# Kernel tuning notes

Measured on AMD Instinct MI355X. Metric: run time of the kernel, lower is better.

## Reference

```python
import jax, jax.numpy as jnp
import numpy as np

B, H, S, D = 2, 16, 2048, 64
NEG = -1e9

def setup_inputs() -> dict:
    key = jax.random.key(0)
    kq, kk, kv, km = jax.random.split(key, 4)
    q = jax.random.normal(kq, (B, H, S, D), dtype=jnp.float32)
    k = jax.random.normal(kk, (B, H, S, D), dtype=jnp.float32)
    v = jax.random.normal(kv, (B, H, S, D), dtype=jnp.float32)
    mask = jax.random.randint(km, (S, S), 0, 2, dtype=jnp.int32)
    return {"q": q, "k": k, "v": v, "mask": mask}

def reference(q, k, v, mask):
    d_k = k.shape[-1]
    temp = jnp.sqrt(jnp.asarray(d_k, q.dtype))  # temperature=None -> sqrt(d_k)
    # scores: [B,H,S,S]
    scores = jnp.einsum('bhqd,bhkd->bhqk', q, k) / temp
    scores = jnp.where(mask == 0, jnp.asarray(NEG, scores.dtype), scores)
    attn = jax.nn.softmax(scores, axis=-1)
    output = jnp.einsum('bhqk,bhkd->bhqd', attn, v)
    return (output, attn)
```

## Files before the change

kernel.cpp:

```cpp
#include <hip/hip_runtime.h>
#include <stdint.h>

#define S 2048
#define D 64
#define NKT (S / 64)
#define SCALEF 0.125f

typedef __attribute__((ext_vector_type(8))) _Float16 half8;
typedef __attribute__((ext_vector_type(4))) float floatx4;
typedef __attribute__((ext_vector_type(4))) unsigned int uint32x4;

__device__ __forceinline__ float redsum16(float x) {
#pragma unroll
  for (int off = 8; off >= 1; off >>= 1) x += __shfl_xor(x, off, 16);
  return x;
}

__global__ __launch_bounds__(256) void conv_k_tiled(const float* __restrict__ k,
                                                    _Float16* __restrict__ kh) {
  __shared__ float tile[64][68];
  int bh = blockIdx.x >> 5;
  int kt = blockIdx.x & 31;
  const floatx4* src4 = (const floatx4*)(k + ((size_t)bh * S + (size_t)kt * 64) * D);
#pragma unroll
  for (int it = 0; it < 4; it++) {
    int idx = threadIdx.x + 256 * it;
    *(floatx4*)&tile[idx >> 4][(idx & 15) * 4] = src4[idx];
  }
  __syncthreads();
  half8* dst = (half8*)(kh + (size_t)(bh * 32 + kt) * 512 * 8);
#pragma unroll
  for (int it = 0; it < 2; it++) {
    int cl = threadIdx.x + 256 * it;
    int quad = cl & 3;
    int r = (cl >> 2) & 63;
    int ch = cl >> 8;
    const float* s = &tile[r][ch * 32 + quad * 8];
    half8 h;
#pragma unroll
    for (int j = 0; j < 8; j++) h[j] = (_Float16)s[j];
    dst[cl] = h;
  }
}

__global__ __launch_bounds__(256) void conv_v_tiled(const float* __restrict__ v,
                                                    _Float16* __restrict__ vt) {
  __shared__ float tile[64][68];
  int bh = blockIdx.x >> 5;
  int kt = blockIdx.x & 31;
  const floatx4* src4 = (const floatx4*)(v + ((size_t)bh * S + (size_t)kt * 64) * D);
#pragma unroll
  for (int it = 0; it < 4; it++) {
    int idx = threadIdx.x + 256 * it;
    *(floatx4*)&tile[idx >> 4][(idx & 15) * 4] = src4[idx];
  }
  __syncthreads();
  half8* dst = (half8*)(vt + (size_t)(bh * 32 + kt) * 512 * 8);
#pragma unroll
  for (int it = 0; it < 2; it++) {
    int cl = threadIdx.x + 256 * it;
    int quad = cl & 3;
    int d = (cl >> 2) & 63;
    int c2 = cl >> 8;
    int kb = c2 * 32 + quad * 8;
    half8 h;
#pragma unroll
    for (int j = 0; j < 8; j++) h[j] = (_Float16)tile[kb + j][d];
    dst[cl] = h;
  }
}

__global__ __launch_bounds__(256) void pack_mask_kernel(const int* __restrict__ mask,
                                                        uint32_t* __restrict__ mp) {
  int i = blockIdx.x * 256 + threadIdx.x;
  int r4 = i & 3;
  int c16 = (i >> 2) & 15;
  int quad = (i >> 6) & 3;
  int kt = (i >> 8) & 31;
  int rt = i >> 13;
  int row = rt * 16 + quad * 4 + r4;
  const int* p = mask + (size_t)row * S + kt * 64 + c16;
  uint32_t b0 = (uint32_t)(p[0] != 0);
  uint32_t b1 = (uint32_t)(p[16] != 0);
  uint32_t b2 = (uint32_t)(p[32] != 0);
  uint32_t b3 = (uint32_t)(p[48] != 0);
  mp[i] = b0 | (b1 << 8) | (b2 << 16) | (b3 << 24);
}

__global__ __launch_bounds__(256, 4) void attn_kernel(
    const float* __restrict__ q, const _Float16* __restrict__ kh,
    const _Float16* __restrict__ vt, const uint32_t* __restrict__ mp,
    float* __restrict__ out_o, float* __restrict__ out_attn) {
  const int bh = blockIdx.x >> 5;
  const int qt = blockIdx.x & 31;
  const int lane = threadIdx.x & 63;
  const int wid = threadIdx.x >> 6;
  const int c16 = lane & 15;
  const int quad = lane >> 4;
  const int rowbase = qt * 64 + wid * 16;

  half8 aq[2];
  {
    const float* qrow = q + ((size_t)bh * S + rowbase + c16) * D + quad * 8;
#pragma unroll
    for (int ch = 0; ch < 2; ch++) {
      const floatx4* p4 = (const floatx4*)(qrow + ch * 32);
      floatx4 f0 = p4[0];
      floatx4 f1 = p4[1];
      half8 h;
      h[0] = (_Float16)(f0[0] * SCALEF); h[1] = (_Float16)(f0[1] * SCALEF);
      h[2] = (_Float16)(f0[2] * SCALEF); h[3] = (_Float16)(f0[3] * SCALEF);
      h[4] = (_Float16)(f1[0] * SCALEF); h[5] = (_Float16)(f1[1] * SCALEF);
      h[6] = (_Float16)(f1[2] * SCALEF); h[7] = (_Float16)(f1[3] * SCALEF);
      aq[ch] = h;
    }
  }

  const _Float16* kbase = kh + ((size_t)bh * 32 * 512 + (size_t)(c16 * 4 + quad)) * 8;
  const _Float16* vbase = vt + ((size_t)bh * 32 * 512 + (size_t)(c16 * 4 + quad)) * 8;
  const uint32x4* mb4 = (const uint32x4*)mp + (size_t)(qt * 4 + wid) * 32 * 64 + lane;

  float l_part[4];
#pragma unroll
  for (int r = 0; r < 4; r++) l_part[r] = 0.0f;

#pragma unroll 1
  for (int kt = 0; kt < NKT; kt++) {
    floatx4 acc[4];
#pragma unroll
    for (int nt = 0; nt < 4; nt++) {
      floatx4 a = {0.0f, 0.0f, 0.0f, 0.0f};
#pragma unroll
      for (int ch = 0; ch < 2; ch++) {
        half8 b = *(const half8*)(kbase + ((size_t)kt * 512 + ch * 256 + nt * 64) * 8);
        a = __builtin_amdgcn_mfma_f32_16x16x32_f16(aq[ch], b, a, 0, 0, 0);
      }
      acc[nt] = a;
    }
    uint32x4 mm = mb4[(size_t)kt * 64];
#pragma unroll
    for (int r = 0; r < 4; r++) {
      uint32_t mb = mm[r];
#pragma unroll
      for (int nt = 0; nt < 4; nt++) {
        float p = ((mb >> (8 * nt)) & 1u) ? __expf(acc[nt][r]) : 0.0f;
        l_part[r] += p;
      }
    }
  }

  float inv_l[4];
#pragma unroll
  for (int r = 0; r < 4; r++) inv_l[r] = 1.0f / redsum16(l_part[r]);

  __shared__ __align__(16) _Float16 plds[2][4][16][72];
  floatx4 oacc[4];
#pragma unroll
  for (int nt = 0; nt < 4; nt++) oacc[nt] = (floatx4){0.0f, 0.0f, 0.0f, 0.0f};

  float* attn_base = out_attn + ((size_t)bh * S + rowbase + 4 * quad) * S + c16;

#pragma unroll 1
  for (int kt = 0; kt < NKT; kt++) {
    floatx4 acc[4];
#pragma unroll
    for (int nt = 0; nt < 4; nt++) {
      floatx4 a = {0.0f, 0.0f, 0.0f, 0.0f};
#pragma unroll
      for (int ch = 0; ch < 2; ch++) {
        half8 b = *(const half8*)(kbase + ((size_t)kt * 512 + ch * 256 + nt * 64) * 8);
        a = __builtin_amdgcn_mfma_f32_16x16x32_f16(aq[ch], b, a, 0, 0, 0);
      }
      acc[nt] = a;
    }
    uint32x4 mm = mb4[(size_t)kt * 64];
    _Float16 (*pb)[72] = plds[kt & 1][wid];
#pragma unroll
    for (int r = 0; r < 4; r++) {
      uint32_t mb = mm[r];
#pragma unroll
      for (int nt = 0; nt < 4; nt++) {
        float sv = acc[nt][r];
        float p = ((mb >> (8 * nt)) & 1u) ? __expf(sv) : 0.0f;
        float av = p * inv_l[r];
        __builtin_nontemporal_store(av, &attn_base[(size_t)r * S + kt * 64 + nt * 16]);
        pb[4 * quad + r][nt * 16 + c16] = (_Float16)av;
      }
    }
    __asm__ volatile("s_waitcnt lgkmcnt(0)" ::: "memory");
    half8 a2[2];
#pragma unroll
    for (int c2 = 0; c2 < 2; c2++)
      a2[c2] = *(const half8*)&pb[c16][c2 * 32 + quad * 8];
#pragma unroll
    for (int nt = 0; nt < 4; nt++) {
      floatx4 o = oacc[nt];
#pragma unroll
      for (int c2 = 0; c2 < 2; c2++) {
        half8 b2 = *(const half8*)(vbase + ((size_t)kt * 512 + c2 * 256 + nt * 64) * 8);
        o = __builtin_amdgcn_mfma_f32_16x16x32_f16(a2[c2], b2, o, 0, 0, 0);
      }
      oacc[nt] = o;
    }
  }

  float* obase = out_o + ((size_t)bh * S + rowbase + 4 * quad) * D + c16;
#pragma unroll
  for (int nt = 0; nt < 4; nt++)
#pragma unroll
    for (int r = 0; r < 4; r++)
      __builtin_nontemporal_store(oacc[nt][r], &obase[(size_t)r * D + nt * 16]);
}

extern "C" void kernel_launch(void* const* d_in, const int* in_sizes, int n_in,
                              void* d_out, int out_size, void* d_ws, size_t ws_size,
                              hipStream_t stream) {
  const float* q = (const float*)d_in[0];
  const float* k = (const float*)d_in[1];
  const float* v = (const float*)d_in[2];
  const int* mask = (const int*)d_in[3];

  char* ws = (char*)d_ws;
  _Float16* kh = (_Float16*)ws;
  _Float16* vt = (_Float16*)(ws + 8388608);
  uint32_t* mp = (uint32_t*)(ws + 16777216);

  float* out_o = (float*)d_out;
  float* out_attn = out_o + (size_t)32 * S * D;

  conv_k_tiled<<<1024, 256, 0, stream>>>(k, kh);
  conv_v_tiled<<<1024, 256, 0, stream>>>(v, vt);
  pack_mask_kernel<<<4096, 256, 0, stream>>>(mask, mp);
  attn_kernel<<<1024, 256, 0, stream>>>(q, kh, vt, mp, out_o, out_attn);
}
```

Baseline: 703.5 us.

## Split key range across two blocks per query tile with atomic reductions

The single attention kernel becomes two kernels. Pass 1 computes row sums and pass 2 computes normalized probabilities and the output. Each query tile is now split across two blocks, each covering half the key tiles, which doubles the grid and raises the occupancy hint to 8. Partial row sums and output accumulators are combined with atomicAdd, so separate zeroing kernels must run first. The output zeroing launch covers more elements than the output holds and spills into the attention buffer, adding redundant memory writes, and the atomics add contention and make the summation order nondeterministic.

```diff
diff --git a/kernel.cpp b/kernel.cpp
--- a/kernel.cpp
+++ b/kernel.cpp
@@ -87,12 +87,16 @@
   mp[i] = b0 | (b1 << 8) | (b2 << 16) | (b3 << 24);
 }
 
-__global__ __launch_bounds__(256, 4) void attn_kernel(
+__global__ __launch_bounds__(256) void zero_kernel(floatx4* __restrict__ p) {
+  p[(size_t)blockIdx.x * 256 + threadIdx.x] = (floatx4){0.0f, 0.0f, 0.0f, 0.0f};
+}
+
+__global__ __launch_bounds__(256, 8) void attn_pass1(
     const float* __restrict__ q, const _Float16* __restrict__ kh,
-    const _Float16* __restrict__ vt, const uint32_t* __restrict__ mp,
-    float* __restrict__ out_o, float* __restrict__ out_attn) {
-  const int bh = blockIdx.x >> 5;
-  const int qt = blockIdx.x & 31;
+    const uint32_t* __restrict__ mp, float* __restrict__ l_ws) {
+  const int half = blockIdx.x & 1;
+  const int qt = (blockIdx.x >> 1) & 31;
+  const int bh = blockIdx.x >> 6;
   const int lane = threadIdx.x & 63;
   const int wid = threadIdx.x >> 6;
   const int c16 = lane & 15;
@@ -117,15 +121,16 @@
   }
 
   const _Float16* kbase = kh + ((size_t)bh * 32 * 512 + (size_t)(c16 * 4 + quad)) * 8;
-  const _Float16* vbase = vt + ((size_t)bh * 32 * 512 + (size_t)(c16 * 4 + quad)) * 8;
   const uint32x4* mb4 = (const uint32x4*)mp + (size_t)(qt * 4 + wid) * 32 * 64 + lane;
 
   float l_part[4];
 #pragma unroll
   for (int r = 0; r < 4; r++) l_part[r] = 0.0f;
 
+  const int kt0 = half * 16;
 #pragma unroll 1
-  for (int kt = 0; kt < NKT; kt++) {
+  for (int kt2 = 0; kt2 < 16; kt2++) {
+    const int kt = kt0 + kt2;
     floatx4 acc[4];
 #pragma unroll
     for (int nt = 0; nt < 4; nt++) {
@@ -149,9 +154,53 @@
     }
   }
 
+#pragma unroll
+  for (int r = 0; r < 4; r++) {
+    float s = redsum16(l_part[r]);
+    if (c16 == 0)
+      atomicAdd(&l_ws[(size_t)bh * S + rowbase + 4 * quad + r], s);
+  }
+}
+
+__global__ __launch_bounds__(256, 8) void attn_pass2(
+    const float* __restrict__ q, const _Float16* __restrict__ kh,
+    const _Float16* __restrict__ vt, const uint32_t* __restrict__ mp,
+    const float* __restrict__ l_ws, float* __restrict__ out_o,
+    float* __restrict__ out_attn) {
+  const int half = blockIdx.x & 1;
+  const int qt = (blockIdx.x >> 1) & 31;
+  const int bh = blockIdx.x >> 6;
+  const int lane = threadIdx.x & 63;
+  const int wid = threadIdx.x >> 6;
+  const int c16 = lane & 15;
+  const int quad = lane >> 4;
+  const int rowbase = qt * 64 + wid * 16;
+
+  half8 aq[2];
+  {
+    const float* qrow = q + ((size_t)bh * S + rowbase + c16) * D + quad * 8;
+#pragma unroll
+    for (int ch = 0; ch < 2; ch++) {
+      const floatx4* p4 = (const floatx4*)(qrow + ch * 32);
+      floatx4 f0 = p4[0];
+      floatx4 f1 = p4[1];
+      half8 h;
+      h[0] = (_Float16)(f0[0] * SCALEF); h[1] = (_Float16)(f0[1] * SCALEF);
+      h[2] = (_Float16)(f0[2] * SCALEF); h[3] = (_Float16)(f0[3] * SCALEF);
+      h[4] = (_Float16)(f1[0] * SCALEF); h[5] = (_Float16)(f1[1] * SCALEF);
+      h[6] = (_Float16)(f1[2] * SCALEF); h[7] = (_Float16)(f1[3] * SCALEF);
+      aq[ch] = h;
+    }
+  }
+
+  const _Float16* kbase = kh + ((size_t)bh * 32 * 512 + (size_t)(c16 * 4 + quad)) * 8;
+  const _Float16* vbase = vt + ((size_t)bh * 32 * 512 + (size_t)(c16 * 4 + quad)) * 8;
+  const uint32x4* mb4 = (const uint32x4*)mp + (size_t)(qt * 4 + wid) * 32 * 64 + lane;
+
   float inv_l[4];
 #pragma unroll
-  for (int r = 0; r < 4; r++) inv_l[r] = 1.0f / redsum16(l_part[r]);
+  for (int r = 0; r < 4; r++)
+    inv_l[r] = 1.0f / l_ws[(size_t)bh * S + rowbase + 4 * quad + r];
 
   __shared__ __align__(16) _Float16 plds[2][4][16][72];
   floatx4 oacc[4];
@@ -160,8 +209,10 @@
 
   float* attn_base = out_attn + ((size_t)bh * S + rowbase + 4 * quad) * S + c16;
 
+  const int kt0 = half * 16;
 #pragma unroll 1
-  for (int kt = 0; kt < NKT; kt++) {
+  for (int kt2 = 0; kt2 < 16; kt2++) {
+    const int kt = kt0 + kt2;
     floatx4 acc[4];
 #pragma unroll
     for (int nt = 0; nt < 4; nt++) {
@@ -174,14 +225,13 @@
       acc[nt] = a;
     }
     uint32x4 mm = mb4[(size_t)kt * 64];
-    _Float16 (*pb)[72] = plds[kt & 1][wid];
+    _Float16 (*pb)[72] = plds[kt2 & 1][wid];
 #pragma unroll
     for (int r = 0; r < 4; r++) {
       uint32_t mb = mm[r];
 #pragma unroll
       for (int nt = 0; nt < 4; nt++) {
-        float sv = acc[nt][r];
-        float p = ((mb >> (8 * nt)) & 1u) ? __expf(sv) : 0.0f;
+        float p = ((mb >> (8 * nt)) & 1u) ? __expf(acc[nt][r]) : 0.0f;
         float av = p * inv_l[r];
         __builtin_nontemporal_store(av, &attn_base[(size_t)r * S + kt * 64 + nt * 16]);
         pb[4 * quad + r][nt * 16 + c16] = (_Float16)av;
@@ -209,7 +259,7 @@
   for (int nt = 0; nt < 4; nt++)
 #pragma unroll
     for (int r = 0; r < 4; r++)
-      __builtin_nontemporal_store(oacc[nt][r], &obase[(size_t)r * D + nt * 16]);
+      atomicAdd(&obase[(size_t)r * D + nt * 16], oacc[nt][r]);
 }
 
 extern "C" void kernel_launch(void* const* d_in, const int* in_sizes, int n_in,
@@ -224,6 +274,7 @@
   _Float16* kh = (_Float16*)ws;
   _Float16* vt = (_Float16*)(ws + 8388608);
   uint32_t* mp = (uint32_t*)(ws + 16777216);
+  float* l_ws = (float*)(ws + 20971520);
 
   float* out_o = (float*)d_out;
   float* out_attn = out_o + (size_t)32 * S * D;
@@ -231,5 +282,8 @@
   conv_k_tiled<<<1024, 256, 0, stream>>>(k, kh);
   conv_v_tiled<<<1024, 256, 0, stream>>>(v, vt);
   pack_mask_kernel<<<4096, 256, 0, stream>>>(mask, mp);
-  attn_kernel<<<1024, 256, 0, stream>>>(q, kh, vt, mp, out_o, out_attn);
-}
+  zero_kernel<<<64, 256, 0, stream>>>((floatx4*)l_ws);
+  zero_kernel<<<16384, 256, 0, stream>>>((floatx4*)out_o);
+  attn_pass1<<<2048, 256, 0, stream>>>(q, kh, mp, l_ws);
+  attn_pass2<<<2048, 256, 0, stream>>>(q, kh, vt, mp, l_ws, out_o, out_attn);
+}
```

New measurement: 767.7 us. 1.09x slower.

## Stage attn tile in LDS for coalesced vector stores, remap blocks, set MFMA priority

Applied to the files above, without the earlier changes.

The probability tile is now written to shared memory in fp32 and read back as float4 rows, so each attention-matrix store is a 16-byte write to consecutive columns instead of scattered scalar stores. The fp16 A-operand for the PV MFMA is rebuilt from that same fp32 staging buffer. Block indices are remapped so that eight heads share a query tile in neighbouring blocks, which should improve mask and cache locality. s_setprio raises wave priority around the MFMA sections. The cost is twice the LDS footprint and extra shared-memory reads and conversions.

```diff
diff --git a/kernel.cpp b/kernel.cpp
--- a/kernel.cpp
+++ b/kernel.cpp
@@ -91,8 +91,9 @@
     const float* __restrict__ q, const _Float16* __restrict__ kh,
     const _Float16* __restrict__ vt, const uint32_t* __restrict__ mp,
     float* __restrict__ out_o, float* __restrict__ out_attn) {
-  const int bh = blockIdx.x >> 5;
-  const int qt = blockIdx.x & 31;
+  const int bid = blockIdx.x;
+  const int qt = (bid >> 3) & 31;
+  const int bh = (bid & 7) + 8 * (bid >> 8);
   const int lane = threadIdx.x & 63;
   const int wid = threadIdx.x >> 6;
   const int c16 = lane & 15;
@@ -127,6 +128,7 @@
 #pragma unroll 1
   for (int kt = 0; kt < NKT; kt++) {
     floatx4 acc[4];
+    __builtin_amdgcn_s_setprio(1);
 #pragma unroll
     for (int nt = 0; nt < 4; nt++) {
       floatx4 a = {0.0f, 0.0f, 0.0f, 0.0f};
@@ -137,6 +139,7 @@
       }
       acc[nt] = a;
     }
+    __builtin_amdgcn_s_setprio(0);
     uint32x4 mm = mb4[(size_t)kt * 64];
 #pragma unroll
     for (int r = 0; r < 4; r++) {
@@ -153,16 +156,19 @@
 #pragma unroll
   for (int r = 0; r < 4; r++) inv_l[r] = 1.0f / redsum16(l_part[r]);
 
-  __shared__ __align__(16) _Float16 plds[2][4][16][72];
+  __shared__ __align__(16) float sst[2][4][16][68];
   floatx4 oacc[4];
 #pragma unroll
   for (int nt = 0; nt < 4; nt++) oacc[nt] = (floatx4){0.0f, 0.0f, 0.0f, 0.0f};
 
-  float* attn_base = out_attn + ((size_t)bh * S + rowbase + 4 * quad) * S + c16;
+  const int srow = lane >> 4;
+  const int scol = (lane & 15) * 4;
+  float* attn_srow_base = out_attn + ((size_t)bh * S + rowbase) * S;
 
 #pragma unroll 1
   for (int kt = 0; kt < NKT; kt++) {
     floatx4 acc[4];
+    __builtin_amdgcn_s_setprio(1);
 #pragma unroll
     for (int nt = 0; nt < 4; nt++) {
       floatx4 a = {0.0f, 0.0f, 0.0f, 0.0f};
@@ -173,25 +179,38 @@
       }
       acc[nt] = a;
     }
+    __builtin_amdgcn_s_setprio(0);
     uint32x4 mm = mb4[(size_t)kt * 64];
-    _Float16 (*pb)[72] = plds[kt & 1][wid];
+    float (*sb)[68] = sst[kt & 1][wid];
 #pragma unroll
     for (int r = 0; r < 4; r++) {
       uint32_t mb = mm[r];
 #pragma unroll
       for (int nt = 0; nt < 4; nt++) {
-        float sv = acc[nt][r];
-        float p = ((mb >> (8 * nt)) & 1u) ? __expf(sv) : 0.0f;
-        float av = p * inv_l[r];
-        __builtin_nontemporal_store(av, &attn_base[(size_t)r * S + kt * 64 + nt * 16]);
-        pb[4 * quad + r][nt * 16 + c16] = (_Float16)av;
+        float p = ((mb >> (8 * nt)) & 1u) ? __expf(acc[nt][r]) : 0.0f;
+        sb[4 * quad + r][nt * 16 + c16] = p * inv_l[r];
       }
     }
     __asm__ volatile("s_waitcnt lgkmcnt(0)" ::: "memory");
+#pragma unroll
+    for (int g = 0; g < 4; g++) {
+      floatx4 vv = *(const floatx4*)&sb[g * 4 + srow][scol];
+      __builtin_nontemporal_store(
+          vv, (floatx4*)(attn_srow_base + (size_t)(g * 4 + srow) * S + kt * 64 + scol));
+    }
     half8 a2[2];
 #pragma unroll
-    for (int c2 = 0; c2 < 2; c2++)
-      a2[c2] = *(const half8*)&pb[c16][c2 * 32 + quad * 8];
+    for (int c2 = 0; c2 < 2; c2++) {
+      floatx4 lo = *(const floatx4*)&sb[c16][c2 * 32 + quad * 8];
+      floatx4 hi = *(const floatx4*)&sb[c16][c2 * 32 + quad * 8 + 4];
+      half8 h;
+      h[0] = (_Float16)lo[0]; h[1] = (_Float16)lo[1];
+      h[2] = (_Float16)lo[2]; h[3] = (_Float16)lo[3];
+      h[4] = (_Float16)hi[0]; h[5] = (_Float16)hi[1];
+      h[6] = (_Float16)hi[2]; h[7] = (_Float16)hi[3];
+      a2[c2] = h;
+    }
+    __builtin_amdgcn_s_setprio(1);
 #pragma unroll
     for (int nt = 0; nt < 4; nt++) {
       floatx4 o = oacc[nt];
@@ -202,6 +221,7 @@
       }
       oacc[nt] = o;
     }
+    __builtin_amdgcn_s_setprio(0);
   }
 
   float* obase = out_o + ((size_t)bh * S + rowbase + 4 * quad) * D + c16;
```

Measured after the change: 693.5 us. About the same (-1.4%).
